# Optimization experiments

Hardware: AMD Instinct MI355X
Metric: run time of the kernel (lower is better)

## Reference

```python
import jax, jax.numpy as jnp
import numpy as np

B, S, D = 4, 2048, 1024

def _xavier(key, shape):
    bound = float(np.sqrt(6.0 / (shape[0] + shape[1])))
    return jax.random.uniform(key, shape, dtype=jnp.float32, minval=-bound, maxval=bound)

def setup_inputs() -> dict:
    key = jax.random.key(0)
    k0, k1, k2, k3 = jax.random.split(key, 4)
    return {
        "embeddings": jax.random.normal(k0, (B, S, D), dtype=jnp.float32),
        "W_Q": _xavier(k1, (D, D)),
        "W_K": _xavier(k2, (D, D)),
        "W_V": _xavier(k3, (D, D)),
    }

def reference(embeddings, W_Q, W_K, W_V):
    _, seq_len, d = embeddings.shape
    Q = embeddings @ W_Q                      # [B,S,D]
    K = embeddings @ W_K
    V = embeddings @ W_V
    scale = 1.0 / jnp.sqrt(jnp.float32(d))
    scores = jnp.einsum('bqd,bkd->bqk', Q, K) * scale   # [B,S,S]
    causal = jnp.tril(jnp.ones((seq_len, seq_len), dtype=bool))
    scores = jnp.where(causal[None, :, :], scores, -jnp.inf)
    probs = jax.nn.softmax(scores, axis=-1)
    return jnp.einsum('bqk,bkd->bqd', probs, V)
```

## Files before the change

kernel.cpp:

```cpp
#include <hip/hip_runtime.h>
#include <hip/hip_bf16.h>

#define BSZ 4
#define SEQ 2048
#define DIM 1024

typedef __attribute__((ext_vector_type(8))) short bf16x8;
typedef __attribute__((ext_vector_type(4))) float floatx4;

__device__ __forceinline__ unsigned short f2bf(float x) {
  union { float f; unsigned int u; } v; v.f = x;
  unsigned int r = v.u + 0x7fffu + ((v.u >> 16) & 1u);
  return (unsigned short)(r >> 16);
}

template <typename T> __device__ __forceinline__ void store_c(T* p, float v);
template <> __device__ __forceinline__ void store_c<float>(float* p, float v) { *p = v; }
template <> __device__ __forceinline__ void store_c<unsigned short>(unsigned short* p, float v) { *p = f2bf(v); }

__global__ __launch_bounds__(256) void cast_e(const float* __restrict__ in,
                                              unsigned short* __restrict__ out, int n) {
  int i = (blockIdx.x * 256 + threadIdx.x) * 4;
  if (i >= n) return;
  float4 v = *(const float4*)(in + i);
  ushort4 o;
  o.x = f2bf(v.x); o.y = f2bf(v.y); o.z = f2bf(v.z); o.w = f2bf(v.w);
  *(ushort4*)(out + i) = o;
}

__global__ __launch_bounds__(256) void transpose_w(const float* __restrict__ Wq,
                                                   const float* __restrict__ Wk,
                                                   const float* __restrict__ Wv,
                                                   unsigned short* __restrict__ WtQK,
                                                   unsigned short* __restrict__ WtV) {
  __shared__ float tile[32][33];
  int z = blockIdx.z;
  const float* W = (z == 0) ? Wq : (z == 1) ? Wk : Wv;
  unsigned short* dst = (z == 2) ? WtV : WtQK;
  int row_off = (z == 1) ? 1024 : 0;
  int n0 = blockIdx.x * 32, k0 = blockIdx.y * 32;
  int tx = threadIdx.x, ty = threadIdx.y;
  for (int r = ty; r < 32; r += 8)
    tile[r][tx] = W[(size_t)(k0 + r) * DIM + n0 + tx];
  __syncthreads();
  for (int r = ty; r < 32; r += 8)
    dst[(size_t)(row_off + n0 + r) * DIM + k0 + tx] = f2bf(tile[tx][r]);
}

__device__ __forceinline__ void gload16(const unsigned short* g, unsigned short* l) {
  __builtin_amdgcn_global_load_lds(
      (const __attribute__((address_space(1))) unsigned int*)g,
      (__attribute__((address_space(3))) unsigned int*)l, 16, 0, 0);
}

#define NT_PROJ 32

__global__ __launch_bounds__(512, 2) void proj256(
    const unsigned short* __restrict__ Ebf,
    const unsigned short* __restrict__ WtQK,
    const unsigned short* __restrict__ WtV,
    unsigned short* __restrict__ QKo,
    unsigned short* __restrict__ Vt) {
  const unsigned short *A, *B;
  unsigned short* C;
  int ldc, m0, n0;
  int x = blockIdx.x;
  if (x < 256) {
    m0 = (x >> 3) * 256; n0 = (x & 7) * 256;
    A = Ebf; B = WtQK; C = QKo; ldc = 2 * DIM;
  } else {
    x -= 256;
    m0 = (x >> 5) * 256; n0 = (x & 31) * 256;
    A = WtV; B = Ebf; C = Vt; ldc = BSZ * SEQ;
  }

  __shared__ __align__(16) unsigned short sA[4][256][32];
  __shared__ __align__(16) unsigned short sB[4][256][32];

  const int tid = threadIdx.x;
  const int lane = tid & 63;
  const int wid = tid >> 6;
  const int wm = (wid >> 2) * 128;
  const int wn = (wid & 3) * 64;
  const int lr = lane & 15, lq = lane >> 4;

  const unsigned short* gA = A + (size_t)(m0 + (tid >> 2)) * DIM + (tid & 3) * 8;
  const unsigned short* gB = B + (size_t)(n0 + (tid >> 2)) * DIM + (tid & 3) * 8;
  unsigned short* lA = &sA[0][16 * wid][0];
  unsigned short* lB = &sB[0][16 * wid][0];
  const size_t swG = (size_t)128 * DIM;

#define STAGE_A(T) do { int rb_ = (T) & 3; \
    gload16(gA + (size_t)(T) * 32,       lA + rb_ * 8192); \
    gload16(gA + (size_t)(T) * 32 + swG, lA + rb_ * 8192 + 4096); } while (0)
#define STAGE_B(T) do { int rb_ = (T) & 3; \
    gload16(gB + (size_t)(T) * 32,       lB + rb_ * 8192); \
    gload16(gB + (size_t)(T) * 32 + swG, lB + rb_ * 8192 + 4096); } while (0)

  floatx4 acc[8][4] = {};

  STAGE_A(0); STAGE_B(0);
  STAGE_A(1); STAGE_B(1);
  STAGE_A(2); STAGE_B(2);
  asm volatile("s_waitcnt vmcnt(8)" ::: "memory");
  __builtin_amdgcn_s_barrier();

#pragma unroll 1
  for (int T = 0; T < NT_PROJ; ++T) {
    asm volatile("" ::: "memory");
    const int rb = T & 3;
    bf16x8 af[4], bfr[4];
#pragma unroll
    for (int j = 0; j < 4; ++j) bfr[j] = *(const bf16x8*)&sB[rb][wn + j * 16 + lr][lq * 8];
#pragma unroll
    for (int i = 0; i < 4; ++i) af[i] = *(const bf16x8*)&sA[rb][wm + i * 16 + lr][lq * 8];
    if (T + 3 < NT_PROJ) STAGE_A(T + 3);
    __builtin_amdgcn_s_barrier();
    __builtin_amdgcn_s_setprio(1);
#pragma unroll
    for (int i = 0; i < 4; ++i)
#pragma unroll
      for (int j = 0; j < 4; ++j)
        acc[i][j] = __builtin_amdgcn_mfma_f32_16x16x32_bf16(af[i], bfr[j], acc[i][j], 0, 0, 0);
    __builtin_amdgcn_s_setprio(0);
    __builtin_amdgcn_s_barrier();
#pragma unroll
    for (int i = 0; i < 4; ++i) af[i] = *(const bf16x8*)&sA[rb][wm + 64 + i * 16 + lr][lq * 8];
    if (T + 3 < NT_PROJ) STAGE_B(T + 3);
    __builtin_amdgcn_s_barrier();
    __builtin_amdgcn_s_setprio(1);
#pragma unroll
    for (int i = 0; i < 4; ++i)
#pragma unroll
      for (int j = 0; j < 4; ++j)
        acc[4 + i][j] = __builtin_amdgcn_mfma_f32_16x16x32_bf16(af[i], bfr[j], acc[4 + i][j], 0, 0, 0);
    __builtin_amdgcn_s_setprio(0);
    if (T < NT_PROJ - 3)       { asm volatile("s_waitcnt vmcnt(8)" ::: "memory"); }
    else if (T == NT_PROJ - 3) { asm volatile("s_waitcnt vmcnt(4)" ::: "memory"); }
    else if (T == NT_PROJ - 2) { asm volatile("s_waitcnt vmcnt(0)" ::: "memory"); }
    else                       { asm volatile("" ::: "memory"); }
    __builtin_amdgcn_s_barrier();
  }
#undef STAGE_A
#undef STAGE_B

#pragma unroll
  for (int i = 0; i < 8; ++i) {
    int rbase = m0 + wm + i * 16 + lq * 4;
#pragma unroll
    for (int j = 0; j < 4; ++j) {
      int col = n0 + wn + j * 16 + lr;
#pragma unroll
      for (int r = 0; r < 4; ++r)
        C[(size_t)(rbase + r) * ldc + col] = f2bf(acc[i][j][r]);
    }
  }
}

template <typename OutT, int MODE>
__global__ __launch_bounds__(256) void gemm_nt(
    const unsigned short* __restrict__ A, int lda, long long strideA,
    const unsigned short* __restrict__ B, int ldb, long long strideB,
    OutT* __restrict__ C, int ldc, long long strideC,
    int Kdim, float scale, float* __restrict__ rowsum) {
  int m0, n0;
  if constexpr (MODE == 1) {
    int t = blockIdx.x;
    int mt = 0;
    while (((mt + 1) * (mt + 2)) / 2 <= t) mt++;
    int nt = t - (mt * (mt + 1)) / 2;
    m0 = mt * 128; n0 = nt * 128;
  } else {
    m0 = (gridDim.y - 1 - blockIdx.y) * 128;
    n0 = blockIdx.x * 128;
  }
  int Keff = (MODE == 2) ? min(Kdim, m0 + 128) : Kdim;
  A += (long long)blockIdx.z * strideA;
  B += (long long)blockIdx.z * strideB;
  C += (long long)blockIdx.z * strideC;
  rowsum += (size_t)blockIdx.z * SEQ;

  __shared__ __align__(16) unsigned short As[128][72];
  __shared__ __align__(16) unsigned short Bs[128][72];

  int tid = threadIdx.x;
  int lane = tid & 63;
  int wid = tid >> 6;
  int wm = (wid >> 1) * 64, wn = (wid & 1) * 64;
  int lr = lane & 15, lq = lane >> 4;
  int row = tid >> 3;
  int kc = (tid & 7) * 8;

  const unsigned short* Ab = A + (size_t)(m0 + row) * lda + kc;
  const unsigned short* Bb = B + (size_t)(n0 + row) * ldb + kc;
  size_t la = (size_t)32 * lda, lb = (size_t)32 * ldb;

  uint4 ra0 = *(const uint4*)(Ab);
  uint4 ra1 = *(const uint4*)(Ab + la);
  uint4 ra2 = *(const uint4*)(Ab + 2 * la);
  uint4 ra3 = *(const uint4*)(Ab + 3 * la);
  uint4 rb0 = *(const uint4*)(Bb);
  uint4 rb1 = *(const uint4*)(Bb + lb);
  uint4 rb2 = *(const uint4*)(Bb + 2 * lb);
  uint4 rb3 = *(const uint4*)(Bb + 3 * lb);

  floatx4 acc[4][4] = {};

  for (int k0 = 0; k0 < Keff; k0 += 64) {
    __syncthreads();
    *(uint4*)&As[row][kc]      = ra0;
    *(uint4*)&As[row + 32][kc] = ra1;
    *(uint4*)&As[row + 64][kc] = ra2;
    *(uint4*)&As[row + 96][kc] = ra3;
    *(uint4*)&Bs[row][kc]      = rb0;
    *(uint4*)&Bs[row + 32][kc] = rb1;
    *(uint4*)&Bs[row + 64][kc] = rb2;
    *(uint4*)&Bs[row + 96][kc] = rb3;
    if (k0 + 64 < Keff) {
      const unsigned short* An = Ab + k0 + 64;
      const unsigned short* Bn = Bb + k0 + 64;
      ra0 = *(const uint4*)(An);
      ra1 = *(const uint4*)(An + la);
      ra2 = *(const uint4*)(An + 2 * la);
      ra3 = *(const uint4*)(An + 3 * la);
      rb0 = *(const uint4*)(Bn);
      rb1 = *(const uint4*)(Bn + lb);
      rb2 = *(const uint4*)(Bn + 2 * lb);
      rb3 = *(const uint4*)(Bn + 3 * lb);
    }
    __syncthreads();
#pragma unroll
    for (int kk = 0; kk < 64; kk += 32) {
      bf16x8 af[4], bfr[4];
      int kl = kk + lq * 8;
#pragma unroll
      for (int i = 0; i < 4; i++) af[i] = *(const bf16x8*)&As[wm + i * 16 + lr][kl];
#pragma unroll
      for (int j = 0; j < 4; j++) bfr[j] = *(const bf16x8*)&Bs[wn + j * 16 + lr][kl];
#pragma unroll
      for (int i = 0; i < 4; i++)
#pragma unroll
        for (int j = 0; j < 4; j++)
          acc[i][j] = __builtin_amdgcn_mfma_f32_16x16x32_bf16(af[i], bfr[j], acc[i][j], 0, 0, 0);
    }
  }

  if constexpr (MODE == 1) {
#pragma unroll
    for (int i = 0; i < 4; i++) {
      int rbase = m0 + wm + i * 16 + lq * 4;
      float s0 = 0.f, s1 = 0.f, s2 = 0.f, s3 = 0.f;
#pragma unroll
      for (int j = 0; j < 4; j++) {
        int col = n0 + wn + j * 16 + lr;
        float e0 = (col <= rbase + 0) ? __expf(acc[i][j][0] * scale) : 0.0f;
        float e1 = (col <= rbase + 1) ? __expf(acc[i][j][1] * scale) : 0.0f;
        float e2 = (col <= rbase + 2) ? __expf(acc[i][j][2] * scale) : 0.0f;
        float e3 = (col <= rbase + 3) ? __expf(acc[i][j][3] * scale) : 0.0f;
        store_c(&C[(size_t)(rbase + 0) * ldc + col], e0);
        store_c(&C[(size_t)(rbase + 1) * ldc + col], e1);
        store_c(&C[(size_t)(rbase + 2) * ldc + col], e2);
        store_c(&C[(size_t)(rbase + 3) * ldc + col], e3);
        s0 += e0; s1 += e1; s2 += e2; s3 += e3;
      }
#pragma unroll
      for (int m = 1; m < 16; m <<= 1) {
        s0 += __shfl_xor(s0, m, 64);
        s1 += __shfl_xor(s1, m, 64);
        s2 += __shfl_xor(s2, m, 64);
        s3 += __shfl_xor(s3, m, 64);
      }
      if (lr == 0) {
        atomicAdd(&rowsum[rbase + 0], s0);
        atomicAdd(&rowsum[rbase + 1], s1);
        atomicAdd(&rowsum[rbase + 2], s2);
        atomicAdd(&rowsum[rbase + 3], s3);
      }
    }
  } else {
#pragma unroll
    for (int i = 0; i < 4; i++) {
      int rbase = m0 + wm + i * 16 + lq * 4;
      float i0 = 1.0f / rowsum[rbase + 0];
      float i1 = 1.0f / rowsum[rbase + 1];
      float i2 = 1.0f / rowsum[rbase + 2];
      float i3 = 1.0f / rowsum[rbase + 3];
#pragma unroll
      for (int j = 0; j < 4; j++) {
        int col = n0 + wn + j * 16 + lr;
        store_c(&C[(size_t)(rbase + 0) * ldc + col], acc[i][j][0] * i0);
        store_c(&C[(size_t)(rbase + 1) * ldc + col], acc[i][j][1] * i1);
        store_c(&C[(size_t)(rbase + 2) * ldc + col], acc[i][j][2] * i2);
        store_c(&C[(size_t)(rbase + 3) * ldc + col], acc[i][j][3] * i3);
      }
    }
  }
}

extern "C" void kernel_launch(void* const* d_in, const int* in_sizes, int n_in,
                              void* d_out, int out_size, void* d_ws, size_t ws_size,
                              hipStream_t stream) {
  const float* E  = (const float*)d_in[0];
  const float* Wq = (const float*)d_in[1];
  const float* Wk = (const float*)d_in[2];
  const float* Wv = (const float*)d_in[3];
  float* out = (float*)d_out;

  char* ws = (char*)d_ws;
  size_t off = 0;
  auto alloc = [&](size_t bytes) {
    void* p = ws + off;
    off += (bytes + 255) & ~(size_t)255;
    return p;
  };
  const size_t M_ALL = (size_t)BSZ * SEQ;
  unsigned short* Ebf  = (unsigned short*)alloc(M_ALL * DIM * 2);
  unsigned short* WtQK = (unsigned short*)alloc((size_t)2 * DIM * DIM * 2);
  unsigned short* WtV  = (unsigned short*)alloc((size_t)DIM * DIM * 2);
  unsigned short* QK   = (unsigned short*)alloc(M_ALL * 2 * DIM * 2);
  unsigned short* Vt   = (unsigned short*)alloc((size_t)DIM * M_ALL * 2);
  unsigned short* ExpS = (unsigned short*)alloc((size_t)BSZ * SEQ * SEQ * 2);
  float*          Rsum = (float*)alloc((size_t)BSZ * SEQ * 4);

  int nE = (int)(M_ALL * DIM);
  cast_e<<<dim3(nE / (256 * 4)), dim3(256), 0, stream>>>(E, Ebf, nE);
  transpose_w<<<dim3(32, 32, 3), dim3(32, 8), 0, stream>>>(Wq, Wk, Wv, WtQK, WtV);
  hipMemsetAsync(Rsum, 0, (size_t)BSZ * SEQ * 4, stream);

  proj256<<<dim3(384), dim3(512), 0, stream>>>(Ebf, WtQK, WtV, QK, Vt);

  gemm_nt<unsigned short, 1><<<dim3(136, 1, BSZ), dim3(256), 0, stream>>>(
      QK, 2 * DIM, (long long)SEQ * 2 * DIM,
      QK + DIM, 2 * DIM, (long long)SEQ * 2 * DIM,
      ExpS, SEQ, (long long)SEQ * SEQ,
      DIM, 0.03125f , Rsum);

  gemm_nt<float, 2><<<dim3(8, 16, BSZ), dim3(256), 0, stream>>>(
      ExpS, SEQ, (long long)SEQ * SEQ,
      Vt, (int)M_ALL, (long long)SEQ,
      out, DIM, (long long)SEQ * DIM,
      SEQ, 1.0f, Rsum);
}
```

Before: 258.8 us.

## Split V projection into 128-row tiles, add XOR LDS swizzle, unroll loop

```diff
diff --git a/kernel.cpp b/kernel.cpp
--- a/kernel.cpp
+++ b/kernel.cpp
@@ -55,105 +55,128 @@
 
 #define NT_PROJ 32
 
+template <int BMt>
+__device__ __forceinline__ void proj_core(
+    const unsigned short* __restrict__ A,
+    const unsigned short* __restrict__ Bm,
+    unsigned short* __restrict__ C, int ldc, int m0, int n0,
+    unsigned short* sAr, unsigned short* sBr) {
+  constexpr int LPA = BMt / 128;
+  constexpr int LPT = LPA + 2;
+  constexpr int FR  = BMt / 32;
+  constexpr int TA  = BMt * 32;
+  constexpr int TB  = 256 * 32;
+
+  const int tid = threadIdx.x;
+  const int lane = tid & 63;
+  const int wid = tid >> 6;
+  const int wm = (wid >> 2) * (BMt / 2);
+  const int wn = (wid & 3) * 64;
+  const int lr = lane & 15, lq = lane >> 4;
+
+  const int srow = tid >> 2;
+  const int schunk = (tid & 3) ^ ((tid >> 3) & 3);
+  const unsigned short* gA = A + (size_t)(m0 + srow) * DIM + schunk * 8;
+  const unsigned short* gB = Bm + (size_t)(n0 + srow) * DIM + schunk * 8;
+  unsigned short* lA = sAr + 16 * 32 * wid;
+  unsigned short* lB = sBr + 16 * 32 * wid;
+  const size_t swG = (size_t)128 * DIM;
+
+#define STAGE_A(T) do { int rb_ = (T) & 3; \
+    gload16(gA + (size_t)(T) * 32, lA + rb_ * TA); \
+    if constexpr (LPA == 2) gload16(gA + (size_t)(T) * 32 + swG, lA + rb_ * TA + 4096); } while (0)
+#define STAGE_B(T) do { int rb_ = (T) & 3; \
+    gload16(gB + (size_t)(T) * 32,       lB + rb_ * TB); \
+    gload16(gB + (size_t)(T) * 32 + swG, lB + rb_ * TB + 4096); } while (0)
+#define ARD(rb_, rowv) (*(const bf16x8*)&sAr[(rb_) * TA + (rowv) * 32 + (lq ^ (((rowv) >> 1) & 3)) * 8])
+#define BRD(rb_, rowv) (*(const bf16x8*)&sBr[(rb_) * TB + (rowv) * 32 + (lq ^ (((rowv) >> 1) & 3)) * 8])
+
+  floatx4 acc[FR][4] = {};
+
+  STAGE_A(0); STAGE_B(0);
+  STAGE_A(1); STAGE_B(1);
+  STAGE_A(2); STAGE_B(2);
+  if constexpr (LPT == 4) asm volatile("s_waitcnt vmcnt(8)" ::: "memory");
+  else                    asm volatile("s_waitcnt vmcnt(6)" ::: "memory");
+  __builtin_amdgcn_s_barrier();
+
+#pragma unroll 4
+  for (int T = 0; T < NT_PROJ; ++T) {
+    const int rb = T & 3;
+    bf16x8 af[4], bfr[4];
+#pragma unroll
+    for (int j = 0; j < 4; ++j) bfr[j] = BRD(rb, wn + j * 16 + lr);
+#pragma unroll
+    for (int i = 0; i < 4; ++i) af[i] = ARD(rb, wm + i * 16 + lr);
+    if (T + 3 < NT_PROJ) {
+      STAGE_A(T + 3);
+      if constexpr (BMt == 128) STAGE_B(T + 3);
+    }
+    __builtin_amdgcn_s_barrier();
+    __builtin_amdgcn_s_setprio(1);
+#pragma unroll
+    for (int i = 0; i < 4; ++i)
+#pragma unroll
+      for (int j = 0; j < 4; ++j)
+        acc[i][j] = __builtin_amdgcn_mfma_f32_16x16x32_bf16(af[i], bfr[j], acc[i][j], 0, 0, 0);
+    __builtin_amdgcn_s_setprio(0);
+    if constexpr (BMt == 256) {
+      __builtin_amdgcn_s_barrier();
+#pragma unroll
+      for (int i = 0; i < 4; ++i) af[i] = ARD(rb, wm + 64 + i * 16 + lr);
+      if (T + 3 < NT_PROJ) STAGE_B(T + 3);
+      __builtin_amdgcn_s_barrier();
+      __builtin_amdgcn_s_setprio(1);
+#pragma unroll
+      for (int i = 0; i < 4; ++i)
+#pragma unroll
+        for (int j = 0; j < 4; ++j)
+          acc[4 + i][j] = __builtin_amdgcn_mfma_f32_16x16x32_bf16(af[i], bfr[j], acc[4 + i][j], 0, 0, 0);
+      __builtin_amdgcn_s_setprio(0);
+    }
+    if (T < NT_PROJ - 3) {
+      if constexpr (LPT == 4) asm volatile("s_waitcnt vmcnt(8)" ::: "memory");
+      else                    asm volatile("s_waitcnt vmcnt(6)" ::: "memory");
+    } else if (T == NT_PROJ - 3) {
+      if constexpr (LPT == 4) asm volatile("s_waitcnt vmcnt(4)" ::: "memory");
+      else                    asm volatile("s_waitcnt vmcnt(3)" ::: "memory");
+    } else if (T == NT_PROJ - 2) {
+      asm volatile("s_waitcnt vmcnt(0)" ::: "memory");
+    }
+    __builtin_amdgcn_s_barrier();
+  }
+#undef STAGE_A
+#undef STAGE_B
+#undef ARD
+#undef BRD
+
+#pragma unroll
+  for (int i = 0; i < FR; ++i) {
+    int rbase = m0 + wm + i * 16 + lq * 4;
+#pragma unroll
+    for (int j = 0; j < 4; ++j) {
+      int col = n0 + wn + j * 16 + lr;
+#pragma unroll
+      for (int r = 0; r < 4; ++r)
+        C[(size_t)(rbase + r) * ldc + col] = f2bf(acc[i][j][r]);
+    }
+  }
+}
+
 __global__ __launch_bounds__(512, 2) void proj256(
     const unsigned short* __restrict__ Ebf,
     const unsigned short* __restrict__ WtQK,
     const unsigned short* __restrict__ WtV,
     unsigned short* __restrict__ QKo,
     unsigned short* __restrict__ Vt) {
-  const unsigned short *A, *B;
-  unsigned short* C;
-  int ldc, m0, n0;
+  __shared__ __align__(16) unsigned short sA[4 * 256 * 32];
+  __shared__ __align__(16) unsigned short sB[4 * 256 * 32];
   int x = blockIdx.x;
   if (x < 256) {
-    m0 = (x >> 3) * 256; n0 = (x & 7) * 256;
-    A = Ebf; B = WtQK; C = QKo; ldc = 2 * DIM;
+    proj_core<256>(Ebf, WtQK, QKo, 2 * DIM, (x >> 3) * 256, (x & 7) * 256, sA, sB);
   } else {
     x -= 256;
-    m0 = (x >> 5) * 256; n0 = (x & 31) * 256;
-    A = WtV; B = Ebf; C = Vt; ldc = BSZ * SEQ;
-  }
-
-  __shared__ __align__(16) unsigned short sA[4][256][32];
-  __shared__ __align__(16) unsigned short sB[4][256][32];
-
-  const int tid = threadIdx.x;
-  const int lane = tid & 63;
-  const int wid = tid >> 6;
-  const int wm = (wid >> 2) * 128;
-  const int wn = (wid & 3) * 64;
-  const int lr = lane & 15, lq = lane >> 4;
-
-  const unsigned short* gA = A + (size_t)(m0 + (tid >> 2)) * DIM + (tid & 3) * 8;
-  const unsigned short* gB = B + (size_t)(n0 + (tid >> 2)) * DIM + (tid & 3) * 8;
-  unsigned short* lA = &sA[0][16 * wid][0];
-  unsigned short* lB = &sB[0][16 * wid][0];
-  const size_t swG = (size_t)128 * DIM;
-
-#define STAGE_A(T) do { int rb_ = (T) & 3; \
-    gload16(gA + (size_t)(T) * 32,       lA + rb_ * 8192); \
-    gload16(gA + (size_t)(T) * 32 + swG, lA + rb_ * 8192 + 4096); } while (0)
-#define STAGE_B(T) do { int rb_ = (T) & 3; \
-    gload16(gB + (size_t)(T) * 32,       lB + rb_ * 8192); \
-    gload16(gB + (size_t)(T) * 32 + swG, lB + rb_ * 8192 + 4096); } while (0)
-
-  floatx4 acc[8][4] = {};
-
-  STAGE_A(0); STAGE_B(0);
-  STAGE_A(1); STAGE_B(1);
-  STAGE_A(2); STAGE_B(2);
-  asm volatile("s_waitcnt vmcnt(8)" ::: "memory");
-  __builtin_amdgcn_s_barrier();
-
-#pragma unroll 1
-  for (int T = 0; T < NT_PROJ; ++T) {
-    asm volatile("" ::: "memory");
-    const int rb = T & 3;
-    bf16x8 af[4], bfr[4];
-#pragma unroll
-    for (int j = 0; j < 4; ++j) bfr[j] = *(const bf16x8*)&sB[rb][wn + j * 16 + lr][lq * 8];
-#pragma unroll
-    for (int i = 0; i < 4; ++i) af[i] = *(const bf16x8*)&sA[rb][wm + i * 16 + lr][lq * 8];
-    if (T + 3 < NT_PROJ) STAGE_A(T + 3);
-    __builtin_amdgcn_s_barrier();
-    __builtin_amdgcn_s_setprio(1);
-#pragma unroll
-    for (int i = 0; i < 4; ++i)
-#pragma unroll
-      for (int j = 0; j < 4; ++j)
-        acc[i][j] = __builtin_amdgcn_mfma_f32_16x16x32_bf16(af[i], bfr[j], acc[i][j], 0, 0, 0);
-    __builtin_amdgcn_s_setprio(0);
-    __builtin_amdgcn_s_barrier();
-#pragma unroll
-    for (int i = 0; i < 4; ++i) af[i] = *(const bf16x8*)&sA[rb][wm + 64 + i * 16 + lr][lq * 8];
-    if (T + 3 < NT_PROJ) STAGE_B(T + 3);
-    __builtin_amdgcn_s_barrier();
-    __builtin_amdgcn_s_setprio(1);
-#pragma unroll
-    for (int i = 0; i < 4; ++i)
-#pragma unroll
-      for (int j = 0; j < 4; ++j)
-        acc[4 + i][j] = __builtin_amdgcn_mfma_f32_16x16x32_bf16(af[i], bfr[j], acc[4 + i][j], 0, 0, 0);
-    __builtin_amdgcn_s_setprio(0);
-    if (T < NT_PROJ - 3)       { asm volatile("s_waitcnt vmcnt(8)" ::: "memory"); }
-    else if (T == NT_PROJ - 3) { asm volatile("s_waitcnt vmcnt(4)" ::: "memory"); }
-    else if (T == NT_PROJ - 2) { asm volatile("s_waitcnt vmcnt(0)" ::: "memory"); }
-    else                       { asm volatile("" ::: "memory"); }
-    __builtin_amdgcn_s_barrier();
-  }
-#undef STAGE_A
-#undef STAGE_B
-
-#pragma unroll
-  for (int i = 0; i < 8; ++i) {
-    int rbase = m0 + wm + i * 16 + lq * 4;
-#pragma unroll
-    for (int j = 0; j < 4; ++j) {
-      int col = n0 + wn + j * 16 + lr;
-#pragma unroll
-      for (int r = 0; r < 4; ++r)
-        C[(size_t)(rbase + r) * ldc + col] = f2bf(acc[i][j][r]);
-    }
+    proj_core<128>(WtV, Ebf, Vt, BSZ * SEQ, (x >> 5) * 128, (x & 31) * 256, sA, sB);
   }
 }
 
@@ -327,7 +350,7 @@
   transpose_w<<<dim3(32, 32, 3), dim3(32, 8), 0, stream>>>(Wq, Wk, Wv, WtQK, WtV);
   hipMemsetAsync(Rsum, 0, (size_t)BSZ * SEQ * 4, stream);
 
-  proj256<<<dim3(384), dim3(512), 0, stream>>>(Ebf, WtQK, WtV, QK, Vt);
+  proj256<<<dim3(512), dim3(512), 0, stream>>>(Ebf, WtQK, WtV, QK, Vt);
 
   gemm_nt<unsigned short, 1><<<dim3(136, 1, BSZ), dim3(256), 0, stream>>>(
       QK, 2 * DIM, (long long)SEQ * 2 * DIM,
```

New measurement: 244.0 us. 5.8% less time.
